# Kernel tuning notes

Hardware: AMD Instinct MI355X
Metric: run time of the kernel (lower is better)

## Reference

```python
import jax, jax.numpy as jnp
import numpy as np

N = 50000      # nodes
E = 800000     # edges (avg degree 16)
D = 128        # in_dim == hidden_dim
CD = 3         # coord_dim (SE(3))
L = 3          # num_layers


def setup_inputs() -> dict:
    key = jax.random.key(0)
    ks = jax.random.split(key, 10)
    s = np.float32(1.0 / np.sqrt(D))
    return {
        "x": jax.random.normal(ks[0], (N, D), jnp.float32),
        "pos": jax.random.normal(ks[1], (N, CD), jnp.float32),
        "edge_index": jax.random.randint(ks[2], (2, E), 0, N, dtype=jnp.int32),
        # per-layer stacked params (in_dim == hidden_dim so all layers stack)
        "Wl": jax.random.normal(ks[3], (L, D, D), jnp.float32) * s,
        "bl": jnp.zeros((L, D), jnp.float32),
        "Wc": jax.random.normal(ks[4], (L, D, 1), jnp.float32) * s,
        "bc": jnp.zeros((L, 1), jnp.float32),
        "WR": jax.random.normal(ks[5], (L, D, CD * CD), jnp.float32) * s,
        "bR": jnp.zeros((L, CD * CD), jnp.float32),
        "Wt": jax.random.normal(ks[6], (L, D, CD), jnp.float32) * s,
        "bt": jnp.zeros((L, CD), jnp.float32),
        # final fc
        "Wf": jax.random.normal(ks[7], (D, D), jnp.float32) * s,
        "bf": jnp.zeros((D,), jnp.float32),
    }


def reference(x, pos, edge_index, Wl, bl, Wc, bc, WR, bR, Wt, bt, Wf, bf):
    src, dst = edge_index[0], edge_index[1]
    n = x.shape[0]
    # R defaults to identity, t to zeros (R_dict/t_dict None path)
    R = jnp.broadcast_to(jnp.eye(CD, dtype=x.dtype), (n, CD, CD))
    t = jnp.zeros_like(pos)
    for i in range(L):
        h = x @ Wl[i] + bl[i]                          # (N, D)  per-edge-type linear
        # MessagePassing aggr='add': message x_j = h[src], scatter-add at dst
        out = jax.ops.segment_sum(h[src], dst, num_segments=n)  # (N, D)
        pos = pos + (out @ Wc[i] + bc[i])              # (N,3) + (N,1) broadcast
        R_upd = (out @ WR[i] + bR[i]).reshape(n, CD, CD)
        Q = jnp.linalg.qr(R_upd)[0]                    # orthonormalize rotation update
        R = Q @ R
        t = t + (out @ Wt[i] + bt[i])
        x = out
    z = x @ Wf + bf
    return z, pos, R, t
```

## Files before the change

kernel.cpp:

```cpp
#include <hip/hip_runtime.h>
#include <hip/hip_fp16.h>

typedef _Float16 half8 __attribute__((ext_vector_type(8)));
typedef float floatx4 __attribute__((ext_vector_type(4)));

#define OSH 13

__device__ inline void qr3_q(const double A[3][3], double Q[3][3]){
  double a[3][3];
#pragma unroll
  for (int r = 0; r < 3; r++)
#pragma unroll
    for (int c = 0; c < 3; c++) a[r][c] = A[r][c];

  double v1[3] = {1.0, 0.0, 0.0};
  double tau1 = 0.0;
  {
    double xn2 = a[1][0]*a[1][0] + a[2][0]*a[2][0];
    if (xn2 != 0.0){
      double alpha = a[0][0];
      double beta = -copysign(sqrt(alpha*alpha + xn2), alpha);
      tau1 = (beta - alpha) / beta;
      double inv = 1.0 / (alpha - beta);
      v1[1] = a[1][0] * inv;
      v1[2] = a[2][0] * inv;
#pragma unroll
      for (int c = 1; c < 3; c++){
        double w = a[0][c] + v1[1]*a[1][c] + v1[2]*a[2][c];
        double tw = tau1 * w;
        a[0][c] -= tw;
        a[1][c] -= tw * v1[1];
        a[2][c] -= tw * v1[2];
      }
    }
  }
  double tau2 = 0.0, v2 = 0.0;
  {
    double x2 = a[2][1];
    if (x2 != 0.0){
      double alpha = a[1][1];
      double beta = -copysign(sqrt(alpha*alpha + x2*x2), alpha);
      tau2 = (beta - alpha) / beta;
      v2 = x2 / (alpha - beta);
    }
  }
  double M[3][3] = {{1.0, 0.0, 0.0},
                    {0.0, 1.0 - tau2, -tau2*v2},
                    {0.0, -tau2*v2, 1.0 - tau2*v2*v2}};
#pragma unroll
  for (int c = 0; c < 3; c++){
    double w = v1[0]*M[0][c] + v1[1]*M[1][c] + v1[2]*M[2][c];
#pragma unroll
    for (int r = 0; r < 3; r++)
      Q[r][c] = M[r][c] - tau1 * v1[r] * w;
  }
}

__device__ inline void se3_node_ds(int n, const float ds[13],
                                   const float* __restrict__ bc, const float* __restrict__ bR,
                                   const float* __restrict__ bt, const float* __restrict__ pos_in,
                                   float* __restrict__ pos_o, float* __restrict__ R_o,
                                   float* __restrict__ t_o, int layer){
  double A[3][3], Q[3][3];
#pragma unroll
  for (int r = 0; r < 3; r++)
#pragma unroll
    for (int c = 0; c < 3; c++)
      A[r][c] = (double)ds[1 + r*3 + c] + (double)bR[r*3 + c];
  qr3_q(A, Q);

  double pd = (double)ds[0] + (double)bc[0];
#pragma unroll
  for (int c = 0; c < 3; c++){
    double base = (layer == 0) ? (double)pos_in[n*3 + c] : (double)pos_o[n*3 + c];
    pos_o[n*3 + c] = (float)(base + pd);
  }

  if (layer == 0){
#pragma unroll
    for (int r = 0; r < 3; r++)
#pragma unroll
      for (int c = 0; c < 3; c++)
        R_o[n*9 + r*3 + c] = (float)Q[r][c];
  } else {
    double Rold[3][3];
#pragma unroll
    for (int r = 0; r < 3; r++)
#pragma unroll
      for (int c = 0; c < 3; c++)
        Rold[r][c] = (double)R_o[n*9 + r*3 + c];
#pragma unroll
    for (int r = 0; r < 3; r++)
#pragma unroll
      for (int c = 0; c < 3; c++){
        double s = Q[r][0]*Rold[0][c] + Q[r][1]*Rold[1][c] + Q[r][2]*Rold[2][c];
        R_o[n*9 + r*3 + c] = (float)s;
      }
  }
#pragma unroll
  for (int c = 0; c < 3; c++){
    double base = (layer == 0) ? 0.0 : (double)t_o[n*3 + c];
    t_o[n*3 + c] = (float)(base + (double)ds[10 + c] + (double)bt[c]);
  }
}

__global__ void k_prep_w(const float* __restrict__ Wl, const float* __restrict__ Wf,
                         const float* __restrict__ Wc, const float* __restrict__ WR,
                         const float* __restrict__ Wt, _Float16* __restrict__ wTx,
                         _Float16* __restrict__ wHd,
                         int* __restrict__ cursor, int nbuck){
  int t = blockIdx.x*256 + threadIdx.x;
  if (blockIdx.x == 0 && threadIdx.x < nbuck) cursor[threadIdx.x] = 0;
  if (t < 4*128*128){
    int l = t >> 14;
    int n = (t >> 7) & 127;
    int k = t & 127;
    const float* W = (l < 3) ? (Wl + (size_t)l*16384) : Wf;
    wTx[t] = (_Float16)W[k*128 + n];
  } else if (t < 4*128*128 + 3*16*128){
    int u = t - 4*128*128;
    int l = u >> 11;
    int r = u & 2047;
    int n = r >> 7;
    int k = r & 127;
    float v = 0.f;
    if (n == 0)      v = Wc[(size_t)l*128 + k];
    else if (n < 10) v = WR[(size_t)l*1152 + k*9 + (n-1)];
    else if (n < 13) v = Wt[(size_t)l*384 + k*3 + (n-10)];
    wHd[u] = (_Float16)v;
  }
}

__launch_bounds__(256)
__global__ void k_cvt(const float* __restrict__ x, _Float16* __restrict__ o, int N){
  int c = blockIdx.x*256 + threadIdx.x;
  if (c >= (N+1)*16) return;
  int n = c >> 4;
  half8 h = {};
  if (n < N){
    const float* p = x + (size_t)c*8;
    float4 f0 = *(const float4*)p;
    float4 f1 = *(const float4*)(p + 4);
    h[0]=(_Float16)f0.x; h[1]=(_Float16)f0.y; h[2]=(_Float16)f0.z; h[3]=(_Float16)f0.w;
    h[4]=(_Float16)f1.x; h[5]=(_Float16)f1.y; h[6]=(_Float16)f1.z; h[7]=(_Float16)f1.w;
  }
  *(half8*)(o + (size_t)c*8) = h;
}

__launch_bounds__(256)
__global__ void k_bin(const int* __restrict__ src, const int* __restrict__ dst,
                      int E, int nbuck, int capB,
                      int* __restrict__ cursor, int* __restrict__ binned){
  __shared__ int cnt[128];
  __shared__ int segbase[128];
  const int tid = threadIdx.x;
  for (int t = tid; t < nbuck; t += 256) cnt[t] = 0;
  __syncthreads();
  const int e0 = blockIdx.x*4096 + tid;
  int pk[16], bk[16];
#pragma unroll
  for (int j = 0; j < 16; j++){
    int e = e0 + j*256;
    if (e < E){
      int d = dst[e], s = src[e];
      bk[j] = d >> 9;
      pk[j] = (s << 9) | (d & 511);
      atomicAdd(&cnt[bk[j]], 1);
    } else bk[j] = -1;
  }
  __syncthreads();
  for (int t = tid; t < nbuck; t += 256){
    int c = cnt[t];
    if (c > 0) segbase[t] = t*capB + atomicAdd(&cursor[t], c);
    cnt[t] = 0;
  }
  __syncthreads();
#pragma unroll
  for (int j = 0; j < 16; j++){
    if (bk[j] >= 0){
      int ord = atomicAdd(&cnt[bk[j]], 1);
      binned[segbase[bk[j]] + ord] = pk[j];
    }
  }
}

__launch_bounds__(256)
__global__ void k_build(const int* __restrict__ binned, const int* __restrict__ cursor,
                        int N, int capB, int capC,
                        int2* __restrict__ sd, int* __restrict__ csr){
  __shared__ int deg2[512*8];
  __shared__ int lst2[512*8];
  __shared__ int cnt2[512*8];
  __shared__ int scn[256];
  const int b = blockIdx.x, tid = threadIdx.x;
  for (int t = tid; t < 512*8; t += 256){ deg2[t] = 0; cnt2[t] = 0; }
  __syncthreads();
  const int nE = cursor[b];
  const int gbase = b*capB;
  for (int i = tid; i < nE; i += 256){
    int v = binned[gbase + i];
    int o = v >> (9 + OSH);
    if (o > 7) o = 7;
    atomicAdd(&deg2[((v & 511) << 3) + o], 1);
  }
  __syncthreads();
  int d0 = 0, d1 = 0;
#pragma unroll
  for (int o = 0; o < 8; o++){ d0 += deg2[((2*tid) << 3) + o]; d1 += deg2[((2*tid+1) << 3) + o]; }
  const int p0 = (d0+7)&~7, p1 = (d1+7)&~7;
  scn[tid] = p0 + p1;
  __syncthreads();
#pragma unroll
  for (int off = 1; off < 256; off <<= 1){
    int add = (tid >= off) ? scn[tid-off] : 0;
    __syncthreads();
    scn[tid] += add;
    __syncthreads();
  }
  const int ex = scn[tid] - (p0 + p1);
  const int csrb = b*capC;
  {
    int off0 = ex;
#pragma unroll
    for (int o = 0; o < 8; o++){ lst2[((2*tid) << 3) + o] = off0; off0 += deg2[((2*tid) << 3) + o]; }
    int off1 = ex + p0;
#pragma unroll
    for (int o = 0; o < 8; o++){ lst2[((2*tid+1) << 3) + o] = off1; off1 += deg2[((2*tid+1) << 3) + o]; }
  }
  const int n0 = b*512 + 2*tid, n1 = n0 + 1;
  if (n0 < N) sd[n0] = make_int2(csrb + ex, (d0 << 16) | p0);
  if (n1 < N) sd[n1] = make_int2(csrb + ex + p0, (d1 << 16) | p1);
  __syncthreads();
  for (int i = tid; i < nE; i += 256){
    int v = binned[gbase + i];
    int dl = v & 511, s = v >> 9;
    int o = s >> OSH; if (o > 7) o = 7;
    int ord = atomicAdd(&cnt2[(dl << 3) + o], 1);
    csr[csrb + lst2[(dl << 3) + o] + ord] = s;
  }
  for (int j = d0; j < p0; j++) csr[csrb + ex + j] = N;
  for (int j = d1; j < p1; j++) csr[csrb + ex + p0 + j] = N;
}

__launch_bounds__(256)
__global__ void k_fused(const _Float16* __restrict__ Xin,
                        const _Float16* __restrict__ Wmain,
                        const _Float16* __restrict__ Whd,
                        const float* __restrict__ bias,
                        const int* __restrict__ csr, const int2* __restrict__ sd,
                        _Float16* __restrict__ Out,
                        int N, int layer,
                        const float* __restrict__ bc, const float* __restrict__ bR,
                        const float* __restrict__ bt, const float* __restrict__ pos_in,
                        float* __restrict__ pos_o, float* __restrict__ R_o,
                        float* __restrict__ t_o){
  __shared__ __align__(16) _Float16 lg[32][136];
  __shared__ __align__(16) float lheads[32*16];
  __shared__ float ldeg[32];

  const int tid  = threadIdx.x;
  const int wave = tid >> 6;
  const int lane = tid & 63;
  const int quad = lane >> 4;
  const int l16  = lane & 15;
  const int rbase0 = blockIdx.x*32;

  {
    const int nbase = rbase0 + wave*8;
    int nn = nbase + (lane & 7);
    int2 sv = (nn < N) ? sd[nn] : make_int2(0, 0);
    const unsigned int* Xu = (const unsigned int*)Xin;
    for (int i = 0; i < 8; i++){
      int s0    = __builtin_amdgcn_readlane(sv.x, i);
      int dpack = __builtin_amdgcn_readlane(sv.y, i);
      int degp  = dpack & 0xffff;
      if (lane == 0) ldeg[wave*8 + i] = (float)(dpack >> 16);
      float acc0 = 0.f, acc1 = 0.f;
      for (int base = 0; base < degp; base += 64){
        int myidx = csr[s0 + base + lane];
        int m = degp - base; m = (m < 64) ? m : 64;
        for (int k = 0; k < m; k += 8){
          unsigned int v[8];
#pragma unroll
          for (int j = 0; j < 8; j++){
            int idx = __builtin_amdgcn_readlane(myidx, k + j);
            v[j] = Xu[(size_t)idx*64 + lane];
          }
#pragma unroll
          for (int j = 0; j < 8; j++){
            float2 f = __half22float2(*(__half2*)&v[j]);
            acc0 += f.x; acc1 += f.y;
          }
        }
      }
      __half2 ho = __floats2half2_rn(acc0, acc1);
      ((unsigned int*)&lg[wave*8 + i][0])[lane] = *(unsigned int*)&ho;
    }
  }
  __syncthreads();

  const int rt = wave & 1;
  const int cq = wave >> 1;
  half8 af[4];
#pragma unroll
  for (int kc = 0; kc < 4; kc++)
    af[kc] = *(const half8*)&lg[rt*16 + l16][kc*32 + quad*8];
  __syncthreads();

  floatx4 acc[4] = {};
#pragma unroll
  for (int kc = 0; kc < 4; kc++)
#pragma unroll
    for (int ct = 0; ct < 4; ct++){
      half8 bf = *(const half8*)(Wmain + (size_t)((cq*4 + ct)*16 + l16)*128 + kc*32 + quad*8);
      acc[ct] = __builtin_amdgcn_mfma_f32_16x16x32_f16(af[kc], bf, acc[ct], 0, 0, 0);
    }

  {
    float dgv[4];
#pragma unroll
    for (int reg = 0; reg < 4; reg++)
      dgv[reg] = ldeg[rt*16 + quad*4 + reg];
#pragma unroll
    for (int ct = 0; ct < 4; ct++){
      int col = (cq*4 + ct)*16 + l16;
      float b = bias[col];
#pragma unroll
      for (int reg = 0; reg < 4; reg++){
        int rl = rt*16 + quad*4 + reg;
        lg[rl][col] = (_Float16)(acc[ct][reg] + b*dgv[reg]);
      }
    }
  }
  __syncthreads();

#pragma unroll
  for (int i = 0; i < 2; i++){
    int idx8 = i*256 + tid;
    int row = idx8 >> 4, c8 = idx8 & 15;
    int gr = rbase0 + row;
    if (gr < N){
      *(half8*)(Out + (size_t)gr*128 + c8*8) = *(const half8*)&lg[row][c8*8];
    } else if (gr == N){
      half8 z = {};
      *(half8*)(Out + (size_t)gr*128 + c8*8) = z;
    }
  }

  if (wave < 2){
    floatx4 hacc = {};
#pragma unroll
    for (int kc = 0; kc < 4; kc++){
      half8 ha = *(const half8*)&lg[wave*16 + l16][kc*32 + quad*8];
      half8 bf = *(const half8*)(Whd + (size_t)l16*128 + kc*32 + quad*8);
      hacc = __builtin_amdgcn_mfma_f32_16x16x32_f16(ha, bf, hacc, 0, 0, 0);
    }
#pragma unroll
    for (int reg = 0; reg < 4; reg++)
      lheads[(wave*16 + quad*4 + reg)*16 + l16] = hacc[reg];
  }
  __syncthreads();

  if (tid < 32){
    int n = rbase0 + tid;
    if (n < N){
      float ds[13];
#pragma unroll
      for (int c = 0; c < 13; c++) ds[c] = lheads[tid*16 + c];
      se3_node_ds(n, ds, bc, bR, bt, pos_in, pos_o, R_o, t_o, layer);
    }
  }
}

__launch_bounds__(256)
__global__ void k_final(const _Float16* __restrict__ X, const _Float16* __restrict__ Wmain,
                        const float* __restrict__ bias, float* __restrict__ Z, int M){
  __shared__ __align__(16) float lf[64][128];
  const int tid  = threadIdx.x;
  const int wave = tid >> 6;
  const int lane = tid & 63;
  const int quad = lane >> 4;
  const int l16  = lane & 15;
  const int rbase0 = blockIdx.x*64;
  const int rbase  = rbase0 + (wave & 1)*32;
  const int cthi = wave >> 1;

  half8 af[4][2];
#pragma unroll
  for (int kc = 0; kc < 4; kc++)
#pragma unroll
    for (int rt = 0; rt < 2; rt++){
      int r = rbase + rt*16 + l16;
      r = (r < M) ? r : (M - 1);
      af[kc][rt] = *(const half8*)(X + (size_t)r*128 + kc*32 + quad*8);
    }

  floatx4 acc[2][4] = {};
#pragma unroll
  for (int kc = 0; kc < 4; kc++)
#pragma unroll
    for (int ct = 0; ct < 4; ct++){
      half8 bf = *(const half8*)(Wmain + (size_t)((cthi*4 + ct)*16 + l16)*128 + kc*32 + quad*8);
      acc[0][ct] = __builtin_amdgcn_mfma_f32_16x16x32_f16(af[kc][0], bf, acc[0][ct], 0, 0, 0);
      acc[1][ct] = __builtin_amdgcn_mfma_f32_16x16x32_f16(af[kc][1], bf, acc[1][ct], 0, 0, 0);
    }

#pragma unroll
  for (int rt = 0; rt < 2; rt++)
#pragma unroll
    for (int ct = 0; ct < 4; ct++){
      int col = (cthi*4 + ct)*16 + l16;
      float b = bias[col];
#pragma unroll
      for (int reg = 0; reg < 4; reg++){
        int rl = (wave & 1)*32 + rt*16 + quad*4 + reg;
        lf[rl][col] = acc[rt][ct][reg] + b;
      }
    }
  __syncthreads();

#pragma unroll
  for (int i = 0; i < 8; i++){
    int idx4 = i*256 + tid;
    int row = idx4 >> 5, c4 = idx4 & 31;
    int gr = rbase0 + row;
    if (gr < M)
      *(float4*)(Z + (size_t)gr*128 + c4*4) = *(const float4*)&lf[row][c4*4];
  }
}

extern "C" void kernel_launch(void* const* d_in, const int* in_sizes, int n_in,
                              void* d_out, int out_size, void* d_ws, size_t ws_size,
                              hipStream_t stream){
  const float* x0  = (const float*)d_in[0];
  const float* pos = (const float*)d_in[1];
  const int*   ei  = (const int*)d_in[2];
  const float* Wl  = (const float*)d_in[3];
  const float* bl  = (const float*)d_in[4];
  const float* Wc  = (const float*)d_in[5];
  const float* bc  = (const float*)d_in[6];
  const float* WR  = (const float*)d_in[7];
  const float* bR  = (const float*)d_in[8];
  const float* Wt  = (const float*)d_in[9];
  const float* bt  = (const float*)d_in[10];
  const float* Wf  = (const float*)d_in[11];
  const float* bf  = (const float*)d_in[12];

  const int N = in_sizes[0] / 128;
  const int E = in_sizes[2] / 2;
  const int* srcp = ei;
  const int* dstp = ei + E;

  float* z_out = (float*)d_out;
  float* pos_o = z_out + (size_t)N*128;
  float* R_o   = pos_o + (size_t)N*3;
  float* t_o   = R_o   + (size_t)N*9;

  const int nbuck = (N + 511) >> 9;
  const int capB  = (((E + nbuck - 1)/nbuck)*5/4 + 256 + 63) & ~63;
  const int capC  = capB + 512*7;

  char* ws = (char*)d_ws;
  size_t off = 0;
  auto alloc = [&](size_t bytes)->char*{
    char* p = ws + off; off += (bytes + 511) & ~(size_t)511; return p;
  };
  _Float16* bufA = (_Float16*)alloc((size_t)(N+1)*128*2);
  _Float16* bufB = (_Float16*)alloc((size_t)(N+1)*128*2);
  _Float16* wTx  = (_Float16*)alloc((size_t)4*128*128*2);
  _Float16* wHd  = (_Float16*)alloc((size_t)3*16*128*2);
  int2*  sd     = (int2*) alloc((size_t)N*8);
  int*   cursor = (int*)  alloc((size_t)nbuck*4);
  int*   binned = (int*)  alloc((size_t)nbuck*capB*4);
  int*   csr    = (int*)  alloc((size_t)nbuck*capC*4);

  const int prep_total = 4*128*128 + 3*16*128;
  k_prep_w<<<dim3((prep_total + 255)/256), dim3(256), 0, stream>>>(
      Wl, Wf, Wc, WR, Wt, wTx, wHd, cursor, nbuck);
  k_bin   <<<dim3((E + 4095)/4096), dim3(256), 0, stream>>>(srcp, dstp, E, nbuck, capB, cursor, binned);
  k_build <<<dim3(nbuck), dim3(256), 0, stream>>>(binned, cursor, N, capB, capC, sd, csr);
  k_cvt   <<<dim3(((N+1)*16 + 255)/256), dim3(256), 0, stream>>>(x0, bufA, N);

  const int fused_blocks = (N + 32) >> 5;
  const int final_blocks = (N + 63) >> 6;

  const _Float16* xin = bufA;
  _Float16* xout = bufB;
  for (int layer = 0; layer < 3; layer++){
    k_fused<<<dim3(fused_blocks), dim3(256), 0, stream>>>(
        xin, wTx + (size_t)layer*16384, wHd + (size_t)layer*2048, bl + (size_t)layer*128,
        csr, sd, xout, N, layer,
        bc + layer, bR + (size_t)layer*9, bt + (size_t)layer*3,
        pos, pos_o, R_o, t_o);
    const _Float16* tmp = xin; xin = xout; xout = (_Float16*)tmp;
  }
  k_final<<<dim3(final_blocks), dim3(256), 0, stream>>>(
      xin, wTx + (size_t)3*16384, bf, z_out, N);
}
```

Baseline: 307.7 us.

## Double fused block to 64 rows and interleave two-node gathers per wave

```diff
diff --git a/kernel.cpp b/kernel.cpp
--- a/kernel.cpp
+++ b/kernel.cpp
@@ -242,7 +242,7 @@
   for (int j = d1; j < p1; j++) csr[csrb + ex + p0 + j] = N;
 }
 
-__launch_bounds__(256)
+__launch_bounds__(512)
 __global__ void k_fused(const _Float16* __restrict__ Xin,
                         const _Float16* __restrict__ Wmain,
                         const _Float16* __restrict__ Whd,
@@ -254,57 +254,87 @@
                         const float* __restrict__ bt, const float* __restrict__ pos_in,
                         float* __restrict__ pos_o, float* __restrict__ R_o,
                         float* __restrict__ t_o){
-  __shared__ __align__(16) _Float16 lg[32][136];
-  __shared__ __align__(16) float lheads[32*16];
-  __shared__ float ldeg[32];
+  __shared__ __align__(16) _Float16 lg[64][136];
+  __shared__ __align__(16) float lheads[64*16];
+  __shared__ float ldeg[64];
 
   const int tid  = threadIdx.x;
   const int wave = tid >> 6;
   const int lane = tid & 63;
   const int quad = lane >> 4;
   const int l16  = lane & 15;
-  const int rbase0 = blockIdx.x*32;
+  const int rbase0 = blockIdx.x*64;
 
   {
     const int nbase = rbase0 + wave*8;
     int nn = nbase + (lane & 7);
     int2 sv = (nn < N) ? sd[nn] : make_int2(0, 0);
     const unsigned int* Xu = (const unsigned int*)Xin;
-    for (int i = 0; i < 8; i++){
-      int s0    = __builtin_amdgcn_readlane(sv.x, i);
-      int dpack = __builtin_amdgcn_readlane(sv.y, i);
-      int degp  = dpack & 0xffff;
-      if (lane == 0) ldeg[wave*8 + i] = (float)(dpack >> 16);
-      float acc0 = 0.f, acc1 = 0.f;
-      for (int base = 0; base < degp; base += 64){
-        int myidx = csr[s0 + base + lane];
-        int m = degp - base; m = (m < 64) ? m : 64;
-        for (int k = 0; k < m; k += 8){
-          unsigned int v[8];
-#pragma unroll
-          for (int j = 0; j < 8; j++){
-            int idx = __builtin_amdgcn_readlane(myidx, k + j);
-            v[j] = Xu[(size_t)idx*64 + lane];
+    for (int i = 0; i < 8; i += 2){
+      int s0A = __builtin_amdgcn_readlane(sv.x, i);
+      int dpA = __builtin_amdgcn_readlane(sv.y, i);
+      int s0B = __builtin_amdgcn_readlane(sv.x, i+1);
+      int dpB = __builtin_amdgcn_readlane(sv.y, i+1);
+      int degA = dpA & 0xffff, degB = dpB & 0xffff;
+      if (lane == 0){
+        ldeg[wave*8 + i]     = (float)(dpA >> 16);
+        ldeg[wave*8 + i + 1] = (float)(dpB >> 16);
+      }
+      float a0 = 0.f, a1 = 0.f, b0 = 0.f, b1 = 0.f;
+      int maxd = degA > degB ? degA : degB;
+      for (int base = 0; base < maxd; base += 64){
+        int idxA = 0, idxB = 0;
+        if (base < degA) idxA = csr[s0A + base + lane];
+        if (base < degB) idxB = csr[s0B + base + lane];
+        int mA = degA - base; mA = mA < 0 ? 0 : (mA > 64 ? 64 : mA);
+        int mB = degB - base; mB = mB < 0 ? 0 : (mB > 64 ? 64 : mB);
+        int mM = mA > mB ? mA : mB;
+        for (int k = 0; k < mM; k += 8){
+          unsigned int vA[8], vB[8];
+          if (k < mA){
+#pragma unroll
+            for (int j = 0; j < 8; j++){
+              int idx = __builtin_amdgcn_readlane(idxA, k + j);
+              vA[j] = Xu[(size_t)idx*64 + lane];
+            }
           }
-#pragma unroll
-          for (int j = 0; j < 8; j++){
-            float2 f = __half22float2(*(__half2*)&v[j]);
-            acc0 += f.x; acc1 += f.y;
+          if (k < mB){
+#pragma unroll
+            for (int j = 0; j < 8; j++){
+              int idx = __builtin_amdgcn_readlane(idxB, k + j);
+              vB[j] = Xu[(size_t)idx*64 + lane];
+            }
+          }
+          if (k < mA){
+#pragma unroll
+            for (int j = 0; j < 8; j++){
+              float2 f = __half22float2(*(__half2*)&vA[j]);
+              a0 += f.x; a1 += f.y;
+            }
+          }
+          if (k < mB){
+#pragma unroll
+            for (int j = 0; j < 8; j++){
+              float2 f = __half22float2(*(__half2*)&vB[j]);
+              b0 += f.x; b1 += f.y;
+            }
           }
         }
       }
-      __half2 ho = __floats2half2_rn(acc0, acc1);
-      ((unsigned int*)&lg[wave*8 + i][0])[lane] = *(unsigned int*)&ho;
-    }
-  }
-  __syncthreads();
-
-  const int rt = wave & 1;
-  const int cq = wave >> 1;
+      __half2 hoA = __floats2half2_rn(a0, a1);
+      ((unsigned int*)&lg[wave*8 + i][0])[lane] = *(unsigned int*)&hoA;
+      __half2 hoB = __floats2half2_rn(b0, b1);
+      ((unsigned int*)&lg[wave*8 + i + 1][0])[lane] = *(unsigned int*)&hoB;
+    }
+  }
+  __syncthreads();
+
+  const int rt4 = wave & 3;
+  const int cq  = wave >> 2;
   half8 af[4];
 #pragma unroll
   for (int kc = 0; kc < 4; kc++)
-    af[kc] = *(const half8*)&lg[rt*16 + l16][kc*32 + quad*8];
+    af[kc] = *(const half8*)&lg[rt4*16 + l16][kc*32 + quad*8];
   __syncthreads();
 
   floatx4 acc[4] = {};
@@ -320,14 +350,14 @@
     float dgv[4];
 #pragma unroll
     for (int reg = 0; reg < 4; reg++)
-      dgv[reg] = ldeg[rt*16 + quad*4 + reg];
+      dgv[reg] = ldeg[rt4*16 + quad*4 + reg];
 #pragma unroll
     for (int ct = 0; ct < 4; ct++){
       int col = (cq*4 + ct)*16 + l16;
       float b = bias[col];
 #pragma unroll
       for (int reg = 0; reg < 4; reg++){
-        int rl = rt*16 + quad*4 + reg;
+        int rl = rt4*16 + quad*4 + reg;
         lg[rl][col] = (_Float16)(acc[ct][reg] + b*dgv[reg]);
       }
     }
@@ -336,7 +366,7 @@
 
 #pragma unroll
   for (int i = 0; i < 2; i++){
-    int idx8 = i*256 + tid;
+    int idx8 = i*512 + tid;
     int row = idx8 >> 4, c8 = idx8 & 15;
     int gr = rbase0 + row;
     if (gr < N){
@@ -347,7 +377,7 @@
     }
   }
 
-  if (wave < 2){
+  if (wave < 4){
     floatx4 hacc = {};
 #pragma unroll
     for (int kc = 0; kc < 4; kc++){
@@ -361,7 +391,7 @@
   }
   __syncthreads();
 
-  if (tid < 32){
+  if (tid < 64){
     int n = rbase0 + tid;
     if (n < N){
       float ds[13];
@@ -481,13 +511,13 @@
   k_build <<<dim3(nbuck), dim3(256), 0, stream>>>(binned, cursor, N, capB, capC, sd, csr);
   k_cvt   <<<dim3(((N+1)*16 + 255)/256), dim3(256), 0, stream>>>(x0, bufA, N);
 
-  const int fused_blocks = (N + 32) >> 5;
+  const int fused_blocks = (N + 64) >> 6;
   const int final_blocks = (N + 63) >> 6;
 
   const _Float16* xin = bufA;
   _Float16* xout = bufB;
   for (int layer = 0; layer < 3; layer++){
-    k_fused<<<dim3(fused_blocks), dim3(256), 0, stream>>>(
+    k_fused<<<dim3(fused_blocks), dim3(512), 0, stream>>>(
         xin, wTx + (size_t)layer*16384, wHd + (size_t)layer*2048, bl + (size_t)layer*128,
         csr, sd, xout, N, layer,
         bc + layer, bR + (size_t)layer*9, bt + (size_t)layer*3,
```

Result: faster. 294.8 us (-4.2%).
